# Kernel optimization log

Hardware: AMD Instinct MI355X
Metric: run time of the kernel (lower is better)

## Reference

```python
import jax, jax.numpy as jnp
import numpy as np

N, E, D = 50000, 640000, 128

def _lin_params(key, din, dout, bias=True):
    kw, kb = jax.random.split(key)
    s = 1.0 / np.sqrt(din)
    W = jax.random.uniform(kw, (din, dout), minval=-s, maxval=s, dtype=jnp.float32)
    if bias:
        b = jax.random.uniform(kb, (dout,), minval=-s, maxval=s, dtype=jnp.float32)
        return W, b
    return W

def setup_inputs() -> dict:
    key = jax.random.key(0)
    ks = jax.random.split(key, 12)
    x = jax.random.normal(ks[0], (N, D), dtype=jnp.float32)
    edge_attr = jax.random.normal(ks[1], (E, D), dtype=jnp.float32)
    edge_w = jax.random.uniform(ks[2], (E,), dtype=jnp.float32)
    edge_idx = jax.random.randint(ks[3], (2, E), 0, N, dtype=jnp.int32)
    WA, bA = _lin_params(ks[4], D, D)
    WB, bB = _lin_params(ks[5], D, D)
    WC, bC = _lin_params(ks[6], D, D)
    WD, bD = _lin_params(ks[7], D, D)
    WE, bE = _lin_params(ks[8], D, D)
    W1, b1 = _lin_params(ks[9], D, 2 * D)
    W2, b2 = _lin_params(ks[10], 2 * D, D)
    return {"x": x, "edge_attr": edge_attr, "edge_w": edge_w,
            "WA": WA, "bA": bA, "WB": WB, "bB": bB, "WC": WC, "bC": bC,
            "WD": WD, "bD": bD, "WE": WE, "bE": bE,
            "W1": W1, "b1": b1, "W2": W2, "b2": b2,
            "edge_idx": edge_idx}

def reference(x, edge_attr, edge_w, WA, bA, WB, bB, WC, bC, WD, bD, WE, bE, W1, b1, W2, b2, edge_idx):
    n_nodes = x.shape[0]
    Ax = x @ WA + bA
    Bx = x @ WB + bB
    Ce = edge_attr @ WC + bC
    Dx = x @ WD + bD
    Ex = x @ WE + bE
    row, col = edge_idx[0], edge_idx[1]
    # gated edge messages: e_ij = Dx[row] + Ex[col] + Ce  [E, D]
    e_ij = Dx[row] + Ex[col] + Ce
    msg = edge_w[:, None] * (jax.nn.sigmoid(e_ij) * Bx[col])
    aggr = jax.ops.segment_sum(msg, row, num_segments=n_nodes)
    x_trans = jax.nn.relu(Ax + aggr)
    e_trans = jax.nn.relu(e_ij)
    # residual (identity projection since dims match)
    x_final = x + x_trans
    e_final = edge_attr + e_trans
    # FFN block with residual (no batchnorm, dropout=0)
    x_final = x_final + (jax.nn.relu(x_final @ W1 + b1) @ W2 + b2)
    return (x_final, e_final)
```

## Files before the change

kernel.cpp:

```cpp
#include <hip/hip_runtime.h>
#include <cstdint>
#include <cstddef>


__device__ __forceinline__ float4 ld4(const float* p) { return *reinterpret_cast<const float4*>(p); }

template<bool RELU, bool RES>
__device__ __forceinline__ void gemm128(
    const float* __restrict__ A, int lda, int M, int K, int row0,
    const float* __restrict__ B, int ldb,
    const float* __restrict__ bias,
    const float* __restrict__ res, int ldr,
    float* __restrict__ C, int ldc)
{
    __shared__ float AsT[32][132];
    __shared__ float Bs[32][128];
    const int t  = threadIdx.x;
    const int tx = t & 15, ty = t >> 4;
    float acc[8][8] = {};

    for (int kk = 0; kk < K; kk += 32) {
        #pragma unroll
        for (int i = 0; i < 4; ++i) {
            int idx = t + i * 256;
            int r = idx >> 3, c4 = idx & 7;
            int gr = row0 + r;
            float4 v = make_float4(0.f, 0.f, 0.f, 0.f);
            if (gr < M) v = ld4(A + (size_t)gr * lda + kk + c4 * 4);
            AsT[c4 * 4 + 0][r] = v.x;
            AsT[c4 * 4 + 1][r] = v.y;
            AsT[c4 * 4 + 2][r] = v.z;
            AsT[c4 * 4 + 3][r] = v.w;
        }
        #pragma unroll
        for (int i = 0; i < 4; ++i) {
            int idx = t + i * 256;
            int k = idx >> 5, c4 = idx & 31;
            *reinterpret_cast<float4*>(&Bs[k][c4 * 4]) =
                ld4(B + (size_t)(kk + k) * ldb + c4 * 4);
        }
        __syncthreads();
        #pragma unroll
        for (int k = 0; k < 32; ++k) {
            float4 a0 = *reinterpret_cast<const float4*>(&AsT[k][ty * 4]);
            float4 a1 = *reinterpret_cast<const float4*>(&AsT[k][64 + ty * 4]);
            float4 b0 = *reinterpret_cast<const float4*>(&Bs[k][tx * 4]);
            float4 b1 = *reinterpret_cast<const float4*>(&Bs[k][64 + tx * 4]);
            float a[8] = {a0.x, a0.y, a0.z, a0.w, a1.x, a1.y, a1.z, a1.w};
            float b[8] = {b0.x, b0.y, b0.z, b0.w, b1.x, b1.y, b1.z, b1.w};
            #pragma unroll
            for (int i = 0; i < 8; ++i)
                #pragma unroll
                for (int j = 0; j < 8; ++j)
                    acc[i][j] = fmaf(a[i], b[j], acc[i][j]);
        }
        __syncthreads();
    }

    #pragma unroll
    for (int hi = 0; hi < 2; ++hi) {
        #pragma unroll
        for (int i = 0; i < 4; ++i) {
            int gr = row0 + hi * 64 + ty * 4 + i;
            if (gr >= M) continue;
            #pragma unroll
            for (int hj = 0; hj < 2; ++hj) {
                int c = hj * 64 + tx * 4;
                float4 v;
                v.x = acc[hi * 4 + i][hj * 4 + 0] + bias[c + 0];
                v.y = acc[hi * 4 + i][hj * 4 + 1] + bias[c + 1];
                v.z = acc[hi * 4 + i][hj * 4 + 2] + bias[c + 2];
                v.w = acc[hi * 4 + i][hj * 4 + 3] + bias[c + 3];
                if (RELU) {
                    v.x = fmaxf(v.x, 0.f); v.y = fmaxf(v.y, 0.f);
                    v.z = fmaxf(v.z, 0.f); v.w = fmaxf(v.w, 0.f);
                }
                if (RES) {
                    float4 rv = ld4(res + (size_t)gr * ldr + c);
                    v.x += rv.x; v.y += rv.y; v.z += rv.z; v.w += rv.w;
                }
                *reinterpret_cast<float4*>(&C[(size_t)gr * ldc + c]) = v;
            }
        }
    }
}

__global__ __launch_bounds__(256, 3) void node_gemm4_kernel(
    const float* __restrict__ x,
    const float* __restrict__ WA, const float* __restrict__ bA,
    const float* __restrict__ WB, const float* __restrict__ bB,
    const float* __restrict__ WD, const float* __restrict__ bD,
    const float* __restrict__ WE, const float* __restrict__ bE,
    float* __restrict__ NodeFeat, int N)
{
    int sec = blockIdx.y;
    const float* W = sec == 0 ? WA : sec == 1 ? WB : sec == 2 ? WD : WE;
    const float* b = sec == 0 ? bA : sec == 1 ? bB : sec == 2 ? bD : bE;
    gemm128<false, false>(x, 128, N, 128, blockIdx.x * 128, W, 128, b,
                          nullptr, 0, NodeFeat + (size_t)sec * 128, 512);
}

__global__ __launch_bounds__(256, 3) void ce_kernel(
    const float* __restrict__ edge_attr, const float* __restrict__ WC,
    const float* __restrict__ bC, float* __restrict__ ce_out, int E)
{
    gemm128<false, false>(edge_attr, 128, E, 128, blockIdx.x * 128, WC, 128, bC,
                          nullptr, 0, ce_out, 128);
}

__global__ __launch_bounds__(256, 3) void ffn1_kernel(
    const float* __restrict__ xfp, const float* __restrict__ W1,
    const float* __restrict__ b1, float* __restrict__ h, int N)
{
    int cb = blockIdx.y * 128;
    gemm128<true, false>(xfp, 128, N, 128, blockIdx.x * 128, W1 + cb, 256, b1 + cb,
                         nullptr, 0, h + cb, 256);
}

__global__ __launch_bounds__(256, 3) void ffn2_kernel(
    const float* __restrict__ h, const float* __restrict__ W2,
    const float* __restrict__ b2, const float* __restrict__ xfp,
    float* __restrict__ xout, int N)
{
    gemm128<false, true>(h, 256, N, 256, blockIdx.x * 128, W2, 128, b2,
                         xfp, 128, xout, 128);
}

__global__ __launch_bounds__(256) void edge_apply(
    const float* __restrict__ edge_attr, const float* __restrict__ edge_w,
    const int* __restrict__ rowI, const int* __restrict__ colI,
    const float* __restrict__ NodeFeat,
    float* __restrict__ e_final,
    float* __restrict__ aggr, int E)
{
    const int t  = threadIdx.x;
    const int f  = t & 127;
    const int e0 = blockIdx.x * 8 + (t >> 7);
    #pragma unroll
    for (int i = 0; i < 4; ++i) {
        int e = e0 + i * 2;
        if (e >= E) continue;
        int   r  = rowI[e], c = colI[e];
        float w  = edge_w[e];
        float ce = e_final[(size_t)e * 128 + f];
        float ea = edge_attr[(size_t)e * 128 + f];
        float dx = NodeFeat[(size_t)r * 512 + 256 + f];
        float ex = NodeFeat[(size_t)c * 512 + 384 + f];
        float bx = NodeFeat[(size_t)c * 512 + 128 + f];
        float eij = ce + dx + ex;
        float sg  = 1.f / (1.f + __expf(-eij));
        e_final[(size_t)e * 128 + f] = ea + fmaxf(eij, 0.f);
        atomicAdd(&aggr[(size_t)r * 128 + f], w * sg * bx);
    }
}

__global__ __launch_bounds__(256) void node_combine(
    const float* __restrict__ x, const float* __restrict__ NodeFeat,
    const float* __restrict__ aggr, float* __restrict__ xfp, int N)
{
    int i4 = blockIdx.x * blockDim.x + threadIdx.x;
    if (i4 >= N * 32) return;
    int row = i4 >> 5, c4 = i4 & 31;
    float4 xa = ld4(x + (size_t)i4 * 4);
    float4 ax = ld4(NodeFeat + (size_t)row * 512 + c4 * 4);
    float4 ag = ld4(aggr + (size_t)i4 * 4);
    float4 o;
    o.x = xa.x + fmaxf(ax.x + ag.x, 0.f);
    o.y = xa.y + fmaxf(ax.y + ag.y, 0.f);
    o.z = xa.z + fmaxf(ax.z + ag.z, 0.f);
    o.w = xa.w + fmaxf(ax.w + ag.w, 0.f);
    *reinterpret_cast<float4*>(xfp + (size_t)i4 * 4) = o;
}

extern "C" void kernel_launch(void* const* d_in, const int* in_sizes, int n_in,
                              void* d_out, int out_size, void* d_ws, size_t ws_size,
                              hipStream_t stream)
{
    const float* x         = (const float*)d_in[0];
    const float* edge_attr = (const float*)d_in[1];
    const float* edge_w    = (const float*)d_in[2];
    const float* WA = (const float*)d_in[3];  const float* bA = (const float*)d_in[4];
    const float* WB = (const float*)d_in[5];  const float* bB = (const float*)d_in[6];
    const float* WC = (const float*)d_in[7];  const float* bC = (const float*)d_in[8];
    const float* WD = (const float*)d_in[9];  const float* bD = (const float*)d_in[10];
    const float* WE = (const float*)d_in[11]; const float* bE = (const float*)d_in[12];
    const float* W1 = (const float*)d_in[13]; const float* b1 = (const float*)d_in[14];
    const float* W2 = (const float*)d_in[15]; const float* b2 = (const float*)d_in[16];
    const int*   eidx = (const int*)d_in[17];

    const int N = in_sizes[0] / 128;
    const int E = in_sizes[2];
    const int* rowI = eidx;
    const int* colI = eidx + E;

    float* ws       = (float*)d_ws;
    float* NodeFeat = ws;
    float* aggr     = ws + (size_t)N * 512;
    float* h        = ws + (size_t)N * 640;
    float* xfp      = (float*)d_out;
    float* e_final  = (float*)d_out + (size_t)N * 128;

    const int rowTiles = (N + 127) / 128;

    hipMemsetAsync(aggr, 0, (size_t)N * 128 * sizeof(float), stream);
    node_gemm4_kernel<<<dim3(rowTiles, 4), 256, 0, stream>>>(
        x, WA, bA, WB, bB, WD, bD, WE, bE, NodeFeat, N);
    ce_kernel<<<dim3((E + 127) / 128), 256, 0, stream>>>(
        edge_attr, WC, bC, e_final, E);
    edge_apply<<<dim3((E + 7) / 8), 256, 0, stream>>>(
        edge_attr, edge_w, rowI, colI, NodeFeat, e_final, aggr, E);
    node_combine<<<dim3((N * 32 + 255) / 256), 256, 0, stream>>>(
        x, NodeFeat, aggr, xfp, N);
    ffn1_kernel<<<dim3(rowTiles, 2), 256, 0, stream>>>(xfp, W1, b1, h, N);
    ffn2_kernel<<<dim3(rowTiles, 1), 256, 0, stream>>>(h, W2, b2, xfp, xfp, N);
}
```

Before: 1.269 ms.

## Replace FP32 SIMT GEMMs with split-bf16 MFMA GEMMs using pre-transposed weights

All dense projections move from FP32 FMA tiling to MFMA 16x16x32 bf16 instructions. Each FP32 value is split into high and low bf16 parts and three MFMA products are summed to keep near-FP32 accuracy. Weights are converted and transposed into bf16 hi/lo buffers by small kernels each call, reusing workspace regions (h, NodeFeat) as scratch. A register prefetch of the next A tile is added, and the node GEMMs are fused into wider column blocks. This aims to use the matrix cores, at the cost of 3x MFMA work, extra conversion launches, and a small loss of precision.

```diff
diff --git a/kernel.cpp b/kernel.cpp
--- a/kernel.cpp
+++ b/kernel.cpp
@@ -3,127 +3,205 @@
 #include <cstddef>
 
 
+typedef __attribute__((ext_vector_type(8))) short short8;
+typedef __attribute__((ext_vector_type(4))) float f32x4;
+
 __device__ __forceinline__ float4 ld4(const float* p) { return *reinterpret_cast<const float4*>(p); }
 
-template<bool RELU, bool RES>
-__device__ __forceinline__ void gemm128(
+__device__ __forceinline__ uint32_t pack_bf16x2(float f) {
+    uint32_t u  = __float_as_uint(f);
+    uint32_t hi = (u + 0x7fffu + ((u >> 16) & 1u)) >> 16;
+    float    fh = __uint_as_float(hi << 16);
+    uint32_t v  = __float_as_uint(f - fh);
+    uint32_t lo = (v + 0x7fffu + ((v >> 16) & 1u)) >> 16;
+    return (hi << 16) | (lo & 0xffffu);
+}
+
+template<int NW, bool RELU, bool RES>
+__device__ __forceinline__ void mfma_gemm(
     const float* __restrict__ A, int lda, int M, int K, int row0,
-    const float* __restrict__ B, int ldb,
+    const short* __restrict__ BhT, const short* __restrict__ BlT,
     const float* __restrict__ bias,
     const float* __restrict__ res, int ldr,
     float* __restrict__ C, int ldc)
 {
-    __shared__ float AsT[32][132];
-    __shared__ float Bs[32][128];
-    const int t  = threadIdx.x;
-    const int tx = t & 15, ty = t >> 4;
-    float acc[8][8] = {};
+    __shared__ uint32_t As[64][36];
+    constexpr int NT = NW * 64;
+    constexpr int IT = 512 / NT;
+    const int t    = threadIdx.x;
+    const int lane = t & 63;
+    const int l15  = lane & 15, kg = lane >> 4;
+    const int wsec = (t >> 6) * 64;
+
+    f32x4 acc[4][4] = {};
+    float bv[4];
+    #pragma unroll
+    for (int fn = 0; fn < 4; ++fn) bv[fn] = bias[wsec + fn * 16 + l15];
+
+    float4 vbuf[IT];
+    #pragma unroll
+    for (int i = 0; i < IT; ++i) {
+        int idx = t + i * NT, r = idx >> 3, c4 = idx & 7;
+        int gr = row0 + r;
+        vbuf[i] = (gr < M) ? ld4(A + (size_t)gr * lda + c4 * 4)
+                           : make_float4(0.f, 0.f, 0.f, 0.f);
+    }
 
     for (int kk = 0; kk < K; kk += 32) {
         #pragma unroll
-        for (int i = 0; i < 4; ++i) {
-            int idx = t + i * 256;
-            int r = idx >> 3, c4 = idx & 7;
-            int gr = row0 + r;
-            float4 v = make_float4(0.f, 0.f, 0.f, 0.f);
-            if (gr < M) v = ld4(A + (size_t)gr * lda + kk + c4 * 4);
-            AsT[c4 * 4 + 0][r] = v.x;
-            AsT[c4 * 4 + 1][r] = v.y;
-            AsT[c4 * 4 + 2][r] = v.z;
-            AsT[c4 * 4 + 3][r] = v.w;
-        }
+        for (int i = 0; i < IT; ++i) {
+            int idx = t + i * NT, r = idx >> 3, c4 = idx & 7;
+            uint4 p;
+            p.x = pack_bf16x2(vbuf[i].x); p.y = pack_bf16x2(vbuf[i].y);
+            p.z = pack_bf16x2(vbuf[i].z); p.w = pack_bf16x2(vbuf[i].w);
+            *reinterpret_cast<uint4*>(&As[r][c4 * 4]) = p;
+        }
+        __syncthreads();
+
+        if (kk + 32 < K) {
+            #pragma unroll
+            for (int i = 0; i < IT; ++i) {
+                int idx = t + i * NT, r = idx >> 3, c4 = idx & 7;
+                int gr = row0 + r;
+                vbuf[i] = (gr < M) ? ld4(A + (size_t)gr * lda + kk + 32 + c4 * 4)
+                                   : make_float4(0.f, 0.f, 0.f, 0.f);
+            }
+        }
+
+        short8 bh[4], bl[4];
+        #pragma unroll
+        for (int fn = 0; fn < 4; ++fn) {
+            const size_t bo = (size_t)(wsec + fn * 16 + l15) * K + kk + kg * 8;
+            bh[fn] = *reinterpret_cast<const short8*>(BhT + bo);
+            bl[fn] = *reinterpret_cast<const short8*>(BlT + bo);
+        }
+
+        #pragma unroll
+        for (int fm = 0; fm < 4; ++fm) {
+            uint4 a0 = *reinterpret_cast<const uint4*>(&As[fm * 16 + l15][kg * 8]);
+            uint4 a1 = *reinterpret_cast<const uint4*>(&As[fm * 16 + l15][kg * 8 + 4]);
+            short8 ah, al;
+            ah[0] = (short)(a0.x >> 16); al[0] = (short)a0.x;
+            ah[1] = (short)(a0.y >> 16); al[1] = (short)a0.y;
+            ah[2] = (short)(a0.z >> 16); al[2] = (short)a0.z;
+            ah[3] = (short)(a0.w >> 16); al[3] = (short)a0.w;
+            ah[4] = (short)(a1.x >> 16); al[4] = (short)a1.x;
+            ah[5] = (short)(a1.y >> 16); al[5] = (short)a1.y;
+            ah[6] = (short)(a1.z >> 16); al[6] = (short)a1.z;
+            ah[7] = (short)(a1.w >> 16); al[7] = (short)a1.w;
+            #pragma unroll
+            for (int fn = 0; fn < 4; ++fn) {
+                acc[fm][fn] = __builtin_amdgcn_mfma_f32_16x16x32_bf16(ah, bh[fn], acc[fm][fn], 0, 0, 0);
+                acc[fm][fn] = __builtin_amdgcn_mfma_f32_16x16x32_bf16(ah, bl[fn], acc[fm][fn], 0, 0, 0);
+                acc[fm][fn] = __builtin_amdgcn_mfma_f32_16x16x32_bf16(al, bh[fn], acc[fm][fn], 0, 0, 0);
+            }
+        }
+        __syncthreads();
+    }
+
+    #pragma unroll
+    for (int fm = 0; fm < 4; ++fm) {
         #pragma unroll
         for (int i = 0; i < 4; ++i) {
-            int idx = t + i * 256;
-            int k = idx >> 5, c4 = idx & 31;
-            *reinterpret_cast<float4*>(&Bs[k][c4 * 4]) =
-                ld4(B + (size_t)(kk + k) * ldb + c4 * 4);
-        }
-        __syncthreads();
-        #pragma unroll
-        for (int k = 0; k < 32; ++k) {
-            float4 a0 = *reinterpret_cast<const float4*>(&AsT[k][ty * 4]);
-            float4 a1 = *reinterpret_cast<const float4*>(&AsT[k][64 + ty * 4]);
-            float4 b0 = *reinterpret_cast<const float4*>(&Bs[k][tx * 4]);
-            float4 b1 = *reinterpret_cast<const float4*>(&Bs[k][64 + tx * 4]);
-            float a[8] = {a0.x, a0.y, a0.z, a0.w, a1.x, a1.y, a1.z, a1.w};
-            float b[8] = {b0.x, b0.y, b0.z, b0.w, b1.x, b1.y, b1.z, b1.w};
-            #pragma unroll
-            for (int i = 0; i < 8; ++i)
-                #pragma unroll
-                for (int j = 0; j < 8; ++j)
-                    acc[i][j] = fmaf(a[i], b[j], acc[i][j]);
-        }
-        __syncthreads();
-    }
-
-    #pragma unroll
-    for (int hi = 0; hi < 2; ++hi) {
-        #pragma unroll
-        for (int i = 0; i < 4; ++i) {
-            int gr = row0 + hi * 64 + ty * 4 + i;
+            int gr = row0 + fm * 16 + kg * 4 + i;
             if (gr >= M) continue;
             #pragma unroll
-            for (int hj = 0; hj < 2; ++hj) {
-                int c = hj * 64 + tx * 4;
-                float4 v;
-                v.x = acc[hi * 4 + i][hj * 4 + 0] + bias[c + 0];
-                v.y = acc[hi * 4 + i][hj * 4 + 1] + bias[c + 1];
-                v.z = acc[hi * 4 + i][hj * 4 + 2] + bias[c + 2];
-                v.w = acc[hi * 4 + i][hj * 4 + 3] + bias[c + 3];
-                if (RELU) {
-                    v.x = fmaxf(v.x, 0.f); v.y = fmaxf(v.y, 0.f);
-                    v.z = fmaxf(v.z, 0.f); v.w = fmaxf(v.w, 0.f);
-                }
-                if (RES) {
-                    float4 rv = ld4(res + (size_t)gr * ldr + c);
-                    v.x += rv.x; v.y += rv.y; v.z += rv.z; v.w += rv.w;
-                }
-                *reinterpret_cast<float4*>(&C[(size_t)gr * ldc + c]) = v;
+            for (int fn = 0; fn < 4; ++fn) {
+                int col = wsec + fn * 16 + l15;
+                float v = acc[fm][fn][i] + bv[fn];
+                if (RELU) v = fmaxf(v, 0.f);
+                if (RES)  v += res[(size_t)gr * ldr + col];
+                C[(size_t)gr * ldc + col] = v;
             }
         }
     }
 }
 
-__global__ __launch_bounds__(256, 3) void node_gemm4_kernel(
-    const float* __restrict__ x,
-    const float* __restrict__ WA, const float* __restrict__ bA,
-    const float* __restrict__ WB, const float* __restrict__ bB,
-    const float* __restrict__ WD, const float* __restrict__ bD,
-    const float* __restrict__ WE, const float* __restrict__ bE,
+__global__ __launch_bounds__(256) void convert1(
+    const float* __restrict__ WA, const float* __restrict__ WB,
+    const float* __restrict__ WD, const float* __restrict__ WE,
+    const float* __restrict__ WC,
+    const float* __restrict__ bA, const float* __restrict__ bB,
+    const float* __restrict__ bD, const float* __restrict__ bE,
+    short* __restrict__ WcatT_h, short* __restrict__ WcatT_l,
+    short* __restrict__ WCt_h, short* __restrict__ WCt_l,
+    float* __restrict__ bcat)
+{
+    int tid = blockIdx.x * 256 + threadIdx.x;
+    if (tid < 65536) {
+        int k = tid & 127, n = tid >> 7;
+        int sec = n >> 7, nn = n & 127;
+        const float* W = sec == 0 ? WA : sec == 1 ? WB : sec == 2 ? WD : WE;
+        uint32_t p = pack_bf16x2(W[k * 128 + nn]);
+        WcatT_h[n * 128 + k] = (short)(p >> 16);
+        WcatT_l[n * 128 + k] = (short)p;
+    } else if (tid < 81920) {
+        int idx = tid - 65536, k = idx & 127, n = idx >> 7;
+        uint32_t p = pack_bf16x2(WC[k * 128 + n]);
+        WCt_h[n * 128 + k] = (short)(p >> 16);
+        WCt_l[n * 128 + k] = (short)p;
+    } else if (tid < 82432) {
+        int c = tid - 81920, sec = c >> 7;
+        const float* b = sec == 0 ? bA : sec == 1 ? bB : sec == 2 ? bD : bE;
+        bcat[c] = b[c & 127];
+    }
+}
+
+__global__ __launch_bounds__(256) void convert2(
+    const float* __restrict__ W1, const float* __restrict__ W2,
+    short* __restrict__ W1t_h, short* __restrict__ W1t_l,
+    short* __restrict__ W2t_h, short* __restrict__ W2t_l)
+{
+    int tid = blockIdx.x * 256 + threadIdx.x;
+    if (tid < 32768) {
+        int k = tid & 127, n = tid >> 7;
+        uint32_t p = pack_bf16x2(W1[k * 256 + n]);
+        W1t_h[n * 128 + k] = (short)(p >> 16);
+        W1t_l[n * 128 + k] = (short)p;
+    } else if (tid < 65536) {
+        int idx = tid - 32768, k = idx & 255, n = idx >> 8;
+        uint32_t p = pack_bf16x2(W2[k * 128 + n]);
+        W2t_h[n * 256 + k] = (short)(p >> 16);
+        W2t_l[n * 256 + k] = (short)p;
+    }
+}
+
+__global__ __launch_bounds__(256) void node_gemm4_mfma(
+    const float* __restrict__ x, const short* __restrict__ WcatT_h,
+    const short* __restrict__ WcatT_l, const float* __restrict__ bcat,
     float* __restrict__ NodeFeat, int N)
 {
-    int sec = blockIdx.y;
-    const float* W = sec == 0 ? WA : sec == 1 ? WB : sec == 2 ? WD : WE;
-    const float* b = sec == 0 ? bA : sec == 1 ? bB : sec == 2 ? bD : bE;
-    gemm128<false, false>(x, 128, N, 128, blockIdx.x * 128, W, 128, b,
-                          nullptr, 0, NodeFeat + (size_t)sec * 128, 512);
-}
-
-__global__ __launch_bounds__(256, 3) void ce_kernel(
-    const float* __restrict__ edge_attr, const float* __restrict__ WC,
-    const float* __restrict__ bC, float* __restrict__ ce_out, int E)
-{
-    gemm128<false, false>(edge_attr, 128, E, 128, blockIdx.x * 128, WC, 128, bC,
-                          nullptr, 0, ce_out, 128);
-}
-
-__global__ __launch_bounds__(256, 3) void ffn1_kernel(
-    const float* __restrict__ xfp, const float* __restrict__ W1,
-    const float* __restrict__ b1, float* __restrict__ h, int N)
-{
-    int cb = blockIdx.y * 128;
-    gemm128<true, false>(xfp, 128, N, 128, blockIdx.x * 128, W1 + cb, 256, b1 + cb,
-                         nullptr, 0, h + cb, 256);
-}
-
-__global__ __launch_bounds__(256, 3) void ffn2_kernel(
-    const float* __restrict__ h, const float* __restrict__ W2,
-    const float* __restrict__ b2, const float* __restrict__ xfp,
-    float* __restrict__ xout, int N)
-{
-    gemm128<false, true>(h, 256, N, 256, blockIdx.x * 128, W2, 128, b2,
-                         xfp, 128, xout, 128);
+    int col0 = blockIdx.y * 256;
+    mfma_gemm<4, false, false>(x, 128, N, 128, blockIdx.x * 64,
+                               WcatT_h + (size_t)col0 * 128, WcatT_l + (size_t)col0 * 128,
+                               bcat + col0, nullptr, 0, NodeFeat + col0, 512);
+}
+
+__global__ __launch_bounds__(128) void ce_mfma(
+    const float* __restrict__ edge_attr, const short* __restrict__ WCt_h,
+    const short* __restrict__ WCt_l, const float* __restrict__ bC,
+    float* __restrict__ ce_out, int E)
+{
+    mfma_gemm<2, false, false>(edge_attr, 128, E, 128, blockIdx.x * 64,
+                               WCt_h, WCt_l, bC, nullptr, 0, ce_out, 128);
+}
+
+__global__ __launch_bounds__(256) void ffn1_mfma(
+    const float* __restrict__ xfp, const short* __restrict__ W1t_h,
+    const short* __restrict__ W1t_l, const float* __restrict__ b1,
+    float* __restrict__ h, int N)
+{
+    mfma_gemm<4, true, false>(xfp, 128, N, 128, blockIdx.x * 64,
+                              W1t_h, W1t_l, b1, nullptr, 0, h, 256);
+}
+
+__global__ __launch_bounds__(128) void ffn2_mfma(
+    const float* __restrict__ h, const short* __restrict__ W2t_h,
+    const short* __restrict__ W2t_l, const float* __restrict__ b2,
+    const float* __restrict__ xfp, float* __restrict__ xout, int N)
+{
+    mfma_gemm<2, false, true>(h, 256, N, 256, blockIdx.x * 64,
+                              W2t_h, W2t_l, b2, xfp, 128, xout, 128);
 }
 
 __global__ __launch_bounds__(256) void edge_apply(
@@ -200,17 +278,33 @@
     float* xfp      = (float*)d_out;
     float* e_final  = (float*)d_out + (size_t)N * 128;
 
-    const int rowTiles = (N + 127) / 128;
-
+    short* cs      = (short*)h;
+    short* WcatT_h = cs;
+    short* WcatT_l = cs + 65536;
+    short* WCt_h   = cs + 131072;
+    short* WCt_l   = cs + 147456;
+    float* bcat    = h + 81920;
+    short* cs2     = (short*)NodeFeat;
+    short* W1t_h   = cs2;
+    short* W1t_l   = cs2 + 32768;
+    short* W2t_h   = cs2 + 65536;
+    short* W2t_l   = cs2 + 98304;
+
+    const int rowTiles = (N + 63) / 64;
+    const int ceTiles  = (E + 63) / 64;
+
+    convert1<<<dim3(322), 256, 0, stream>>>(WA, WB, WD, WE, WC, bA, bB, bD, bE,
+                                            WcatT_h, WcatT_l, WCt_h, WCt_l, bcat);
     hipMemsetAsync(aggr, 0, (size_t)N * 128 * sizeof(float), stream);
-    node_gemm4_kernel<<<dim3(rowTiles, 4), 256, 0, stream>>>(
-        x, WA, bA, WB, bB, WD, bD, WE, bE, NodeFeat, N);
-    ce_kernel<<<dim3((E + 127) / 128), 256, 0, stream>>>(
-        edge_attr, WC, bC, e_final, E);
+    node_gemm4_mfma<<<dim3(rowTiles, 2), 256, 0, stream>>>(
+        x, WcatT_h, WcatT_l, bcat, NodeFeat, N);
+    ce_mfma<<<dim3(ceTiles), 128, 0, stream>>>(
+        edge_attr, WCt_h, WCt_l, bC, e_final, E);
     edge_apply<<<dim3((E + 7) / 8), 256, 0, stream>>>(
         edge_attr, edge_w, rowI, colI, NodeFeat, e_final, aggr, E);
     node_combine<<<dim3((N * 32 + 255) / 256), 256, 0, stream>>>(
         x, NodeFeat, aggr, xfp, N);
-    ffn1_kernel<<<dim3(rowTiles, 2), 256, 0, stream>>>(xfp, W1, b1, h, N);
-    ffn2_kernel<<<dim3(rowTiles, 1), 256, 0, stream>>>(h, W2, b2, xfp, xfp, N);
-}
+    convert2<<<dim3(256), 256, 0, stream>>>(W1, W2, W1t_h, W1t_l, W2t_h, W2t_l);
+    ffn1_mfma<<<dim3(rowTiles), 256, 0, stream>>>(xfp, W1t_h, W1t_l, b1, h, N);
+    ffn2_mfma<<<dim3(rowTiles), 128, 0, stream>>>(h, W2t_h, W2t_l, b2, xfp, xfp, N);
+}
```

Result: faster. 1.087 ms (-14.4%).
